# Optimization experiments

Measured on AMD Instinct MI355X. Metric: run time of the kernel, lower is better.

Reference implementation:

```python
import jax, jax.numpy as jnp
import numpy as np

BATCH, IN_DIM, GRID, HID, DEPTH = 2048, 128, 128, 256, 7
BN_EPS = 1e-5


def setup_inputs() -> dict:
    key = jax.random.key(0)
    ks = jax.random.split(key, 10)
    x = jax.random.uniform(ks[0], (BATCH, IN_DIM), dtype=jnp.float32)
    grids = jax.random.uniform(ks[1], (DEPTH, IN_DIM, GRID), dtype=jnp.float32)  # torch.rand init
    fs = jax.random.normal(ks[2], (DEPTH, IN_DIM, GRID, HID), dtype=jnp.float32)
    depth_scores = jnp.ones((DEPTH,), dtype=jnp.float32)
    mlp_W = jax.random.normal(ks[3], (3, HID, HID), dtype=jnp.float32) * (1.0 / np.sqrt(HID))
    mlp_b = jnp.zeros((3, HID), dtype=jnp.float32)
    bn_gamma = jnp.ones((3, HID), dtype=jnp.float32)
    bn_beta = jnp.zeros((3, HID), dtype=jnp.float32)
    W_out = jax.random.normal(ks[4], (HID, 1), dtype=jnp.float32) * (1.0 / np.sqrt(HID))
    b_out = jnp.zeros((1,), dtype=jnp.float32)
    return {"x": x, "grids": grids, "fs": fs, "depth_scores": depth_scores,
            "mlp_W": mlp_W, "mlp_b": mlp_b, "bn_gamma": bn_gamma,
            "bn_beta": bn_beta, "W_out": W_out, "b_out": b_out}


def reference(x, grids, fs, depth_scores, mlp_W, mlp_b, bn_gamma, bn_beta, W_out, b_out):
    # per-feature min-max normalization over the batch dim
    xmin = x.min(axis=0, keepdims=True)
    xmax = x.max(axis=0, keepdims=True)
    z = (x - xmin) / (xmax - xmin + 1e-6)  # [B, I]

    outputs = []
    for i in range(DEPTH):
        Bmat = jax.nn.relu(z[:, :, None] - grids[i][None, :, :])  # [B, I, G]
        # (B.unsqueeze(-1) * fs[i]).sum(2).sum(1) == einsum big,igh->bh
        H = jnp.einsum('big,igh->bh', Bmat, fs[i])  # [B, H]
        if i > 0:  # residual accumulation
            H = H + outputs[-1]
        outputs.append(H)
    stacked = jnp.stack(outputs, axis=0)  # [D, B, H]
    w = jax.nn.softmax(depth_scores)  # depth attention
    h = jnp.einsum('d,dbh->bh', w, stacked)

    # MLP head (BatchNorm uses batch stats = training-mode behaviour; Dropout off)
    for j in range(3):
        h = h @ mlp_W[j] + mlp_b[j]
        mean = h.mean(axis=0)
        var = h.var(axis=0)  # biased, matching torch BN normalization
        h = (h - mean) * jax.lax.rsqrt(var + BN_EPS) * bn_gamma[j] + bn_beta[j]
        h = jax.nn.gelu(h, approximate=False)  # torch nn.GELU is exact erf GELU
    return h @ W_out + b_out
```

## Files before the change

kernel.cpp:

```cpp
#include <hip/hip_runtime.h>
#include <hip/hip_bf16.h>

#define BATCH 2048
#define IN_DIM 128
#define GRIDN 128
#define HID 256
#define DEPTH 7

typedef unsigned int u32;
typedef __attribute__((ext_vector_type(8))) short short8;
typedef __attribute__((ext_vector_type(4))) float floatx4;

#define OFF_FST   ((size_t)0)
#define SZ_FST    ((size_t)7*128*256*128*2)
#define OFF_ZT    (OFF_FST + SZ_FST)
#define SZ_ZT     ((size_t)BATCH*IN_DIM*4)
#define OFF_HPRE  (OFF_ZT + SZ_ZT)
#define SZ_HPRE   ((size_t)BATCH*HID*4)
#define OFF_STATS (OFF_HPRE + SZ_HPRE)
#define SZ_STATS  ((size_t)3*2*HID*4)
#define OFF_KEYS  (OFF_STATS + SZ_STATS)
#define SZ_KEYS   ((size_t)256*4)
#define OFF_CW    (OFF_KEYS + SZ_KEYS)
#define SZ_CW     ((size_t)32)
#define OFF_Y1    (OFF_CW + SZ_CW)
#define SZ_Y      ((size_t)BATCH*HID*4)
#define OFF_Y2    (OFF_Y1 + SZ_Y)
#define OFF_Y3    (OFF_Y2 + SZ_Y)

__device__ __forceinline__ void gload_lds16(const void* g, void* l) {
  __builtin_amdgcn_global_load_lds(
      (const __attribute__((address_space(1))) u32*)g,
      (__attribute__((address_space(3))) u32*)l, 16, 0, 0);
}

__device__ __forceinline__ u32 pack2_bf16(float lo, float hi) {
  __hip_bfloat162 b2;
  b2.x = __float2bfloat16(lo);
  b2.y = __float2bfloat16(hi);
  return *reinterpret_cast<u32*>(&b2);
}

__device__ __forceinline__ u32 pk_trunc(float a, float b) {
  return __builtin_amdgcn_perm(__float_as_uint(b), __float_as_uint(a), 0x07060302u);
}

__device__ __forceinline__ float gelu_exact(float x) {
  return 0.5f * x * (1.0f + erff(x * 0.70710678118654752f));
}

__global__ void prep1_kernel(const float* __restrict__ x, u32* __restrict__ keys,
                             const float* __restrict__ depth_scores,
                             float* __restrict__ cw) {
  int t = threadIdx.x;
  int base = blockIdx.x * 256 + t;
  float mn = 1e30f, mx = -1e30f;
#pragma unroll
  for (int j = 0; j < 16; ++j) {
    float v = x[base + j * 16384];
    mn = fminf(mn, v); mx = fmaxf(mx, v);
  }
  __shared__ float smn[256], smx[256];
  smn[t] = mn; smx[t] = mx;
  __syncthreads();
  if (t < 128) {
    mn = fminf(smn[t], smn[t + 128]);
    mx = fmaxf(smx[t], smx[t + 128]);
    int i = base & 127;
    atomicMax(&keys[i], 0x7FFFFFFFu - __float_as_uint(mn));
    atomicMax(&keys[128 + i], __float_as_uint(mx));
  }
  if (blockIdx.x == 0 && t == 0) {
    float m = -1e30f;
    for (int d0 = 0; d0 < DEPTH; ++d0) m = fmaxf(m, depth_scores[d0]);
    float e[DEPTH]; float sum = 0.f;
    for (int d0 = 0; d0 < DEPTH; ++d0) { e[d0] = expf(depth_scores[d0] - m); sum += e[d0]; }
    float cacc = 0.f; float cs[DEPTH];
    for (int d0 = DEPTH - 1; d0 >= 0; --d0) { cacc += e[d0] / sum; cs[d0] = cacc; }
    for (int d0 = 0; d0 < DEPTH; ++d0) cw[d0] = cs[d0];
  }
}

__global__ void prep2_kernel(const float* __restrict__ x, const u32* __restrict__ keys,
                             float* __restrict__ z_t) {
  __shared__ float lds[128 * 65];
  int t = threadIdx.x;
  int b0 = blockIdx.x * 64;
#pragma unroll
  for (int q = 0; q < 32; ++q) {
    int idx = q * 256 + t;
    int b = idx >> 7, i = idx & 127;
    lds[i * 65 + b] = x[(size_t)(b0 + b) * IN_DIM + i];
  }
  __syncthreads();
#pragma unroll
  for (int q = 0; q < 32; ++q) {
    int idx = q * 256 + t;
    int ii = idx >> 6, bb = idx & 63;
    float mnv = __uint_as_float(0x7FFFFFFFu - keys[ii]);
    float mxv = __uint_as_float(keys[128 + ii]);
    float v = (lds[ii * 65 + bb] - mnv) * (1.0f / (mxv - mnv + 1e-6f));
    z_t[(size_t)ii * BATCH + b0 + bb] = v;
  }
}

__global__ void convert_kernel(const float* __restrict__ fs,
                               const float* __restrict__ cw,
                               __hip_bfloat16* __restrict__ fs2) {
  __shared__ u32 lds[256 * 33];
  int slab = blockIdx.x;
  int t = threadIdx.x;
  float cd = cw[slab >> 7];
  const float* src = fs + (size_t)slab * (GRIDN * HID);
  char* dstb = (char*)fs2 + (size_t)slab * 65536;

  for (int gh = 0; gh < 2; ++gh) {
    const float* s0 = src + (size_t)gh * 64 * HID + t;
#pragma unroll
    for (int g2 = 0; g2 < 32; ++g2) {
      float va = s0[(size_t)(2 * g2) * HID];
      float vb = s0[(size_t)(2 * g2 + 1) * HID];
      lds[t * 33 + g2] = pack2_bf16(cd * va, cd * vb);
    }
    __syncthreads();
#pragma unroll
    for (int it2 = 0; it2 < 8; ++it2) {
      int task = t + it2 * 256;
      int c = task >> 9;
      int q = task & 511;
      int nhalf = c >> 1, ksl = c & 1;
      int tt = q >> 6, l4 = (q >> 4) & 3, l15 = q & 15;
      int h = nhalf * 128 + tt * 16 + l15;
      int m = ksl * 4 + l4;
      u32 a0 = lds[h * 33 + m * 4 + 0];
      u32 a1 = lds[h * 33 + m * 4 + 1];
      u32 a2 = lds[h * 33 + m * 4 + 2];
      u32 a3 = lds[h * 33 + m * 4 + 3];
      size_t off = (size_t)nhalf * 32768 + (size_t)(gh * 2 + ksl) * 8192 +
                   (size_t)tt * 1024 + l4 * 256 + l15 * 16;
      *(uint4*)(dstb + off) = make_uint4(a0, a1, a2, a3);
    }
    __syncthreads();
  }
}

__launch_bounds__(256, 2)
__global__ void gemm_kernel(const float* __restrict__ z_t,
                            const float* __restrict__ grids,
                            const __hip_bfloat16* __restrict__ fs2,
                            float* __restrict__ h_pre) {
  __shared__ __align__(16) char lds[65536];

  int bx = blockIdx.x;
  int xcd = bx & 7;
  int t6 = bx >> 3;
  int cg = t6 >> 4;
  int jb = t6 & 15;
  int chunk = xcd + 8 * cg;
  int slab0 = chunk * 28;

  int tid = threadIdx.x;
  int w = tid >> 6, l = tid & 63;
  int l15 = l & 15, l4 = l >> 4;
  int wm = w >> 1;
  int wn = w & 1;
  int mbase = jb * 128 + wm * 64;
  int nbase = wn * 128;
  char* mylds = lds + w * 16384;

  floatx4 acc[4][8];
#pragma unroll
  for (int a = 0; a < 4; ++a)
#pragma unroll
    for (int b = 0; b < 8; ++b) acc[a][b] = (floatx4)0.f;

  const char* fsb = (const char*)fs2 + (size_t)slab0 * 65536 + (size_t)wn * 32768 +
                    (size_t)l * 16;

  auto stage = [&](int step, int p) {
    const char* srcb = fsb + (size_t)(step >> 2) * 65536 + (size_t)(step & 3) * 8192;
    char* dst = mylds + p * 8192;
#pragma unroll
    for (int j = 0; j < 8; ++j)
      gload_lds16(srcb + j * 1024, dst + j * 1024);
  };

  float zv[2][4];
  float4 g0[2], g1[2];
  auto loadzg = [&](int step, int p) {
    int slab = slab0 + (step >> 2);
    int iz = slab & 127;
    const float* zp = z_t + (size_t)iz * BATCH + mbase + l15;
    zv[p][0] = zp[0]; zv[p][1] = zp[16]; zv[p][2] = zp[32]; zv[p][3] = zp[48];
    const float* gp = grids + (size_t)slab * GRIDN + (step & 3) * 32 + l4 * 8;
    g0[p] = *(const float4*)gp;
    g1[p] = *(const float4*)(gp + 4);
  };

  loadzg(0, 0);
  stage(0, 0);

#pragma unroll 2
  for (int step = 0; step < 112; ++step) {
    int p = step & 1;
    __builtin_amdgcn_s_waitcnt(0x0F70);
    __asm__ volatile("" ::: "memory");

    short8 bf[8];
#pragma unroll
    for (int tt = 0; tt < 8; ++tt)
      bf[tt] = *(const short8*)(mylds + p * 8192 + tt * 1024 + l * 16);
    __asm__ volatile("" ::: "memory");

    if (step + 1 < 112) stage(step + 1, p ^ 1);

    short8 af[4];
#pragma unroll
    for (int u = 0; u < 4; ++u) {
      float zu = zv[p][u];
      union { uint4 q; short8 s8; } pk;
      pk.q.x = pk_trunc(fmaxf(zu - g0[p].x, 0.f), fmaxf(zu - g0[p].y, 0.f));
      pk.q.y = pk_trunc(fmaxf(zu - g0[p].z, 0.f), fmaxf(zu - g0[p].w, 0.f));
      pk.q.z = pk_trunc(fmaxf(zu - g1[p].x, 0.f), fmaxf(zu - g1[p].y, 0.f));
      pk.q.w = pk_trunc(fmaxf(zu - g1[p].z, 0.f), fmaxf(zu - g1[p].w, 0.f));
      af[u] = pk.s8;
    }

    if (step + 1 < 112) loadzg(step + 1, p ^ 1);

#pragma unroll
    for (int u = 0; u < 4; ++u)
#pragma unroll
      for (int tt = 0; tt < 8; ++tt)
        acc[u][tt] = __builtin_amdgcn_mfma_f32_16x16x32_bf16(af[u], bf[tt], acc[u][tt], 0, 0, 0);
  }

  int row0 = mbase + l4 * 4;
  int col0 = nbase + l15;
#pragma unroll
  for (int u = 0; u < 4; ++u) {
#pragma unroll
    for (int tt = 0; tt < 8; ++tt) {
      int col = col0 + tt * 16;
#pragma unroll
      for (int r = 0; r < 4; ++r) {
        int row = row0 + u * 16 + r;
        atomicAdd(&h_pre[(size_t)row * HID + col], acc[u][tt][r]);
      }
    }
  }
}

template <int FIRST>
__global__ void mlp_kernel(const float* __restrict__ Xin,
                           const float* __restrict__ statsIn,
                           const float* __restrict__ gamma,
                           const float* __restrict__ beta,
                           const float* __restrict__ W,
                           const float* __restrict__ bias,
                           float* __restrict__ Yout,
                           float* __restrict__ statsOut) {
  __shared__ float Xs[4][HID];
  int br = blockIdx.x, c = threadIdx.x;
  float mean = 0.f, rstd = 1.f, gm = 1.f, bt = 0.f;
  if (!FIRST) {
    float s1 = statsIn[c], s2 = statsIn[HID + c];
    mean = s1 * (1.0f / BATCH);
    float var = s2 * (1.0f / BATCH) - mean * mean;
    rstd = rsqrtf(var + 1e-5f);
    gm = gamma[c]; bt = beta[c];
  }
#pragma unroll
  for (int r = 0; r < 4; ++r) {
    float v = Xin[(size_t)(br * 4 + r) * HID + c];
    if (!FIRST) v = gelu_exact((v - mean) * rstd * gm + bt);
    Xs[r][c] = v;
  }
  __syncthreads();
  float acc[4] = {0, 0, 0, 0};
#pragma unroll 8
  for (int k = 0; k < HID; ++k) {
    float wv = W[(size_t)k * HID + c];
#pragma unroll
    for (int r = 0; r < 4; ++r) acc[r] += Xs[r][k] * wv;
  }
  float bb = bias[c];
  float s1 = 0.f, s2 = 0.f;
#pragma unroll
  for (int r = 0; r < 4; ++r) {
    float y = acc[r] + bb;
    Yout[(size_t)(br * 4 + r) * HID + c] = y;
    s1 += y; s2 += y * y;
  }
  atomicAdd(&statsOut[c], s1);
  atomicAdd(&statsOut[HID + c], s2);
}

__global__ void final_kernel(const float* __restrict__ Y3,
                             const float* __restrict__ statsIn,
                             const float* __restrict__ gamma,
                             const float* __restrict__ beta,
                             const float* __restrict__ W_out,
                             const float* __restrict__ b_out,
                             float* __restrict__ out) {
  int w = threadIdx.x >> 6, l = threadIdx.x & 63;
  int b = blockIdx.x * 4 + w;
  float4 y = *(const float4*)(Y3 + (size_t)b * HID + l * 4);
  float4 wv = *(const float4*)(W_out + l * 4);
  float r4[4] = {y.x, y.y, y.z, y.w};
  float w4[4] = {wv.x, wv.y, wv.z, wv.w};
  float s = 0.f;
  int c0 = l * 4;
#pragma unroll
  for (int q = 0; q < 4; ++q) {
    int c = c0 + q;
    float s1 = statsIn[c], s2 = statsIn[HID + c];
    float mean = s1 * (1.0f / BATCH);
    float var = s2 * (1.0f / BATCH) - mean * mean;
    float rstd = rsqrtf(var + 1e-5f);
    float v = gelu_exact((r4[q] - mean) * rstd * gamma[c] + beta[c]);
    s += v * w4[q];
  }
#pragma unroll
  for (int off = 32; off > 0; off >>= 1) s += __shfl_down(s, off);
  if (l == 0) out[b] = s + b_out[0];
}

extern "C" void kernel_launch(void* const* d_in, const int* in_sizes, int n_in,
                              void* d_out, int out_size, void* d_ws, size_t ws_size,
                              hipStream_t stream) {
  const float* x      = (const float*)d_in[0];
  const float* grids  = (const float*)d_in[1];
  const float* fs     = (const float*)d_in[2];
  const float* dscore = (const float*)d_in[3];
  const float* mlp_W  = (const float*)d_in[4];
  const float* mlp_b  = (const float*)d_in[5];
  const float* bn_g   = (const float*)d_in[6];
  const float* bn_b   = (const float*)d_in[7];
  const float* W_out  = (const float*)d_in[8];
  const float* b_out  = (const float*)d_in[9];
  float* out = (float*)d_out;

  char* ws = (char*)d_ws;
  __hip_bfloat16* fs2 = (__hip_bfloat16*)(ws + OFF_FST);
  float* z_t   = (float*)(ws + OFF_ZT);
  float* h_pre = (float*)(ws + OFF_HPRE);
  float* stats = (float*)(ws + OFF_STATS);
  u32*   keys  = (u32*)(ws + OFF_KEYS);
  float* cw    = (float*)(ws + OFF_CW);
  float* Y1    = (float*)(ws + OFF_Y1);
  float* Y2    = (float*)(ws + OFF_Y2);
  float* Y3    = (float*)(ws + OFF_Y3);

  hipMemsetAsync(h_pre, 0, SZ_HPRE + SZ_STATS + SZ_KEYS, stream);

  prep1_kernel<<<64, 256, 0, stream>>>(x, keys, dscore, cw);
  prep2_kernel<<<32, 256, 0, stream>>>(x, keys, z_t);
  convert_kernel<<<DEPTH * IN_DIM, 256, 0, stream>>>(fs, cw, fs2);
  gemm_kernel<<<512, 256, 0, stream>>>(z_t, grids, fs2, h_pre);

  mlp_kernel<1><<<512, 256, 0, stream>>>(h_pre, nullptr, nullptr, nullptr,
                                         mlp_W, mlp_b, Y1, stats);
  mlp_kernel<0><<<512, 256, 0, stream>>>(Y1, stats, bn_g, bn_b,
                                         mlp_W + 65536, mlp_b + 256, Y2, stats + 512);
  mlp_kernel<0><<<512, 256, 0, stream>>>(Y2, stats + 512, bn_g + 256, bn_b + 256,
                                         mlp_W + 2 * 65536, mlp_b + 2 * 256, Y3, stats + 1024);
  final_kernel<<<512, 256, 0, stream>>>(Y3, stats + 1024, bn_g + 512, bn_b + 512,
                                        W_out, b_out, out);
}
```

Measured before the change: 450.6 us.

## Load GEMM B fragments directly to registers and retile waves as 128x64

The GEMM kernel stops staging fs2 tiles through LDS with global_load_lds. Each wave now loads its bf16 B fragments straight from global memory into registers, double-buffered across k-substeps. The wave tile changes from 64 rows x 128 cols to 128 rows x 64 cols, so each generated A fragment feeds fewer MFMAs while each B fragment is reused across 8 row groups. This removes LDS traffic and waitcnt stalls but relies on global/L2 latency being hidden by register prefetch. The MLP buffers Y1-Y3 are also aliased onto the fs2 region, which is no longer needed once the GEMM has finished.

```diff
diff --git a/kernel.cpp b/kernel.cpp
--- a/kernel.cpp
+++ b/kernel.cpp
@@ -23,16 +23,6 @@
 #define SZ_KEYS   ((size_t)256*4)
 #define OFF_CW    (OFF_KEYS + SZ_KEYS)
 #define SZ_CW     ((size_t)32)
-#define OFF_Y1    (OFF_CW + SZ_CW)
-#define SZ_Y      ((size_t)BATCH*HID*4)
-#define OFF_Y2    (OFF_Y1 + SZ_Y)
-#define OFF_Y3    (OFF_Y2 + SZ_Y)
-
-__device__ __forceinline__ void gload_lds16(const void* g, void* l) {
-  __builtin_amdgcn_global_load_lds(
-      (const __attribute__((address_space(1))) u32*)g,
-      (__attribute__((address_space(3))) u32*)l, 16, 0, 0);
-}
 
 __device__ __forceinline__ u32 pack2_bf16(float lo, float hi) {
   __hip_bfloat162 b2;
@@ -131,11 +121,11 @@
       int nhalf = c >> 1, ksl = c & 1;
       int tt = q >> 6, l4 = (q >> 4) & 3, l15 = q & 15;
       int h = nhalf * 128 + tt * 16 + l15;
-      int m = ksl * 4 + l4;
-      u32 a0 = lds[h * 33 + m * 4 + 0];
-      u32 a1 = lds[h * 33 + m * 4 + 1];
-      u32 a2 = lds[h * 33 + m * 4 + 2];
-      u32 a3 = lds[h * 33 + m * 4 + 3];
+      int mm = ksl * 4 + l4;
+      u32 a0 = lds[h * 33 + mm * 4 + 0];
+      u32 a1 = lds[h * 33 + mm * 4 + 1];
+      u32 a2 = lds[h * 33 + mm * 4 + 2];
+      u32 a3 = lds[h * 33 + mm * 4 + 3];
       size_t off = (size_t)nhalf * 32768 + (size_t)(gh * 2 + ksl) * 8192 +
                    (size_t)tt * 1024 + l4 * 256 + l15 * 16;
       *(uint4*)(dstb + off) = make_uint4(a0, a1, a2, a3);
@@ -144,103 +134,109 @@
   }
 }
 
+#define HALF_GEN_MFMA(U0, gx0, gx1, bfX)                                   \
+  {                                                                        \
+    short8 af[4];                                                          \
+    _Pragma("unroll") for (int uu = 0; uu < 4; ++uu) {                     \
+      float zu = zc[U0 + uu];                                              \
+      union { uint4 q; short8 s8; } pk;                                    \
+      pk.q.x = pk_trunc(fmaxf(zu - gx0.x, 0.f), fmaxf(zu - gx0.y, 0.f));   \
+      pk.q.y = pk_trunc(fmaxf(zu - gx0.z, 0.f), fmaxf(zu - gx0.w, 0.f));   \
+      pk.q.z = pk_trunc(fmaxf(zu - gx1.x, 0.f), fmaxf(zu - gx1.y, 0.f));   \
+      pk.q.w = pk_trunc(fmaxf(zu - gx1.z, 0.f), fmaxf(zu - gx1.w, 0.f));   \
+      af[uu] = pk.s8;                                                      \
+    }                                                                      \
+    _Pragma("unroll") for (int uu = 0; uu < 4; ++uu)                       \
+      _Pragma("unroll") for (int tt = 0; tt < 4; ++tt)                     \
+        acc[U0 + uu][tt] = __builtin_amdgcn_mfma_f32_16x16x32_bf16(        \
+            af[uu], bfX[tt], acc[U0 + uu][tt], 0, 0, 0);                   \
+  }
+
+#define KS_BODY(bfCur, bfNxt, gC0, gC1, gN0, gN1, sN, ksN)                 \
+  {                                                                        \
+    const char* bsrc = bB + (size_t)(sN) * 65536 + (ksN) * 8192;           \
+    bfNxt[0] = *(const short8*)(bsrc);                                     \
+    bfNxt[1] = *(const short8*)(bsrc + 1024);                              \
+    bfNxt[2] = *(const short8*)(bsrc + 2048);                              \
+    bfNxt[3] = *(const short8*)(bsrc + 3072);                              \
+    const float* gp = gG + (size_t)(sN) * GRIDN + (ksN) * 32;              \
+    gN0 = *(const float4*)gp;                                              \
+    gN1 = *(const float4*)(gp + 4);                                        \
+    HALF_GEN_MFMA(0, gC0, gC1, bfCur)                                      \
+    HALF_GEN_MFMA(4, gC0, gC1, bfCur)                                      \
+  }
+
 __launch_bounds__(256, 2)
 __global__ void gemm_kernel(const float* __restrict__ z_t,
                             const float* __restrict__ grids,
                             const __hip_bfloat16* __restrict__ fs2,
                             float* __restrict__ h_pre) {
-  __shared__ __align__(16) char lds[65536];
-
   int bx = blockIdx.x;
   int xcd = bx & 7;
   int t6 = bx >> 3;
   int cg = t6 >> 4;
-  int jb = t6 & 15;
+  int rem = t6 & 15;
+  int mtile = rem >> 1;
+  int nblk = rem & 1;
   int chunk = xcd + 8 * cg;
   int slab0 = chunk * 28;
 
   int tid = threadIdx.x;
   int w = tid >> 6, l = tid & 63;
   int l15 = l & 15, l4 = l >> 4;
-  int wm = w >> 1;
-  int wn = w & 1;
-  int mbase = jb * 128 + wm * 64;
-  int nbase = wn * 128;
-  char* mylds = lds + w * 16384;
-
-  floatx4 acc[4][8];
-#pragma unroll
-  for (int a = 0; a < 4; ++a)
-#pragma unroll
-    for (int b = 0; b < 8; ++b) acc[a][b] = (floatx4)0.f;
-
-  const char* fsb = (const char*)fs2 + (size_t)slab0 * 65536 + (size_t)wn * 32768 +
-                    (size_t)l * 16;
-
-  auto stage = [&](int step, int p) {
-    const char* srcb = fsb + (size_t)(step >> 2) * 65536 + (size_t)(step & 3) * 8192;
-    char* dst = mylds + p * 8192;
-#pragma unroll
-    for (int j = 0; j < 8; ++j)
-      gload_lds16(srcb + j * 1024, dst + j * 1024);
-  };
-
-  float zv[2][4];
-  float4 g0[2], g1[2];
-  auto loadzg = [&](int step, int p) {
-    int slab = slab0 + (step >> 2);
-    int iz = slab & 127;
+  int wm = w >> 1, wn = w & 1;
+  int mbase = mtile * 256 + wm * 128;
+
+  floatx4 acc[8][4];
+#pragma unroll
+  for (int a = 0; a < 8; ++a)
+#pragma unroll
+    for (int b = 0; b < 4; ++b) acc[a][b] = (floatx4)0.f;
+
+  const char* bB = (const char*)fs2 + (size_t)slab0 * 65536 +
+                   (size_t)nblk * 32768 + (size_t)wn * 4096 + (size_t)l * 16;
+  const float* gG = grids + (size_t)slab0 * GRIDN + l4 * 8;
+
+  short8 bfA[4], bfB[4];
+  float4 gA0, gA1, gB0, gB1;
+  float zc[8], zn[8];
+
+  bfA[0] = *(const short8*)(bB);
+  bfA[1] = *(const short8*)(bB + 1024);
+  bfA[2] = *(const short8*)(bB + 2048);
+  bfA[3] = *(const short8*)(bB + 3072);
+  gA0 = *(const float4*)(gG);
+  gA1 = *(const float4*)(gG + 4);
+  {
+    int iz = slab0 & 127;
     const float* zp = z_t + (size_t)iz * BATCH + mbase + l15;
-    zv[p][0] = zp[0]; zv[p][1] = zp[16]; zv[p][2] = zp[32]; zv[p][3] = zp[48];
-    const float* gp = grids + (size_t)slab * GRIDN + (step & 3) * 32 + l4 * 8;
-    g0[p] = *(const float4*)gp;
-    g1[p] = *(const float4*)(gp + 4);
-  };
-
-  loadzg(0, 0);
-  stage(0, 0);
-
-#pragma unroll 2
-  for (int step = 0; step < 112; ++step) {
-    int p = step & 1;
-    __builtin_amdgcn_s_waitcnt(0x0F70);
-    __asm__ volatile("" ::: "memory");
-
-    short8 bf[8];
-#pragma unroll
-    for (int tt = 0; tt < 8; ++tt)
-      bf[tt] = *(const short8*)(mylds + p * 8192 + tt * 1024 + l * 16);
-    __asm__ volatile("" ::: "memory");
-
-    if (step + 1 < 112) stage(step + 1, p ^ 1);
-
-    short8 af[4];
-#pragma unroll
-    for (int u = 0; u < 4; ++u) {
-      float zu = zv[p][u];
-      union { uint4 q; short8 s8; } pk;
-      pk.q.x = pk_trunc(fmaxf(zu - g0[p].x, 0.f), fmaxf(zu - g0[p].y, 0.f));
-      pk.q.y = pk_trunc(fmaxf(zu - g0[p].z, 0.f), fmaxf(zu - g0[p].w, 0.f));
-      pk.q.z = pk_trunc(fmaxf(zu - g1[p].x, 0.f), fmaxf(zu - g1[p].y, 0.f));
-      pk.q.w = pk_trunc(fmaxf(zu - g1[p].z, 0.f), fmaxf(zu - g1[p].w, 0.f));
-      af[u] = pk.s8;
+#pragma unroll
+    for (int u = 0; u < 8; ++u) zc[u] = zp[u * 16];
+  }
+
+#pragma unroll 1
+  for (int s = 0; s < 28; ++s) {
+    int sn = (s + 1 < 28) ? s + 1 : 27;
+    {
+      int iz = (slab0 + sn) & 127;
+      const float* zp = z_t + (size_t)iz * BATCH + mbase + l15;
+#pragma unroll
+      for (int u = 0; u < 8; ++u) zn[u] = zp[u * 16];
     }
-
-    if (step + 1 < 112) loadzg(step + 1, p ^ 1);
-
-#pragma unroll
-    for (int u = 0; u < 4; ++u)
-#pragma unroll
-      for (int tt = 0; tt < 8; ++tt)
-        acc[u][tt] = __builtin_amdgcn_mfma_f32_16x16x32_bf16(af[u], bf[tt], acc[u][tt], 0, 0, 0);
+    KS_BODY(bfA, bfB, gA0, gA1, gB0, gB1, s, 1)
+    KS_BODY(bfB, bfA, gB0, gB1, gA0, gA1, s, 2)
+    KS_BODY(bfA, bfB, gA0, gA1, gB0, gB1, s, 3)
+    KS_BODY(bfB, bfA, gB0, gB1, gA0, gA1, sn, 0)
+#pragma unroll
+    for (int u = 0; u < 8; ++u) zc[u] = zn[u];
   }
 
   int row0 = mbase + l4 * 4;
-  int col0 = nbase + l15;
-#pragma unroll
-  for (int u = 0; u < 4; ++u) {
-#pragma unroll
-    for (int tt = 0; tt < 8; ++tt) {
+  int col0 = nblk * 128 + wn * 64 + l15;
+#pragma unroll
+  for (int u = 0; u < 8; ++u) {
+#pragma unroll
+    for (int tt = 0; tt < 4; ++tt) {
       int col = col0 + tt * 16;
 #pragma unroll
       for (int r = 0; r < 4; ++r) {
@@ -348,9 +344,9 @@
   float* stats = (float*)(ws + OFF_STATS);
   u32*   keys  = (u32*)(ws + OFF_KEYS);
   float* cw    = (float*)(ws + OFF_CW);
-  float* Y1    = (float*)(ws + OFF_Y1);
-  float* Y2    = (float*)(ws + OFF_Y2);
-  float* Y3    = (float*)(ws + OFF_Y3);
+  float* Y1    = (float*)(ws + OFF_FST);
+  float* Y2    = (float*)(ws + OFF_FST + SZ_HPRE);
+  float* Y3    = (float*)(ws + OFF_FST + 2 * SZ_HPRE);
 
   hipMemsetAsync(h_pre, 0, SZ_HPRE + SZ_STATS + SZ_KEYS, stream);
 
```

Measured after the change: 481.0 us. +6.8%, slower.
